# Optimization experiments

Hardware: AMD Instinct MI355X
Metric: run time of the kernel (lower is better)

## Reference

```python
import jax, jax.numpy as jnp
import numpy as np

B, S, HID = 2, 1024, 4096
NH, NKV, HD = 32, 8, 128
GROUPS = NH // NKV  # 4
BITS = 8
SCALING = HD ** -0.5


def quantize_lastdim(x, bits=BITS):
    """Asymmetric min-max fake-quant per row of the last dim (groupsize=-1),
    matching ActQuantizer.find_params + quantize/dequantize."""
    qmax = float(2 ** bits - 1)
    xmin = jnp.minimum(jnp.min(x, axis=-1, keepdims=True), 0.0)
    xmax = jnp.maximum(jnp.max(x, axis=-1, keepdims=True), 0.0)
    rng = xmax - xmin
    scale = jnp.where(rng == 0, 1.0, rng / qmax)
    zero = jnp.round(-xmin / scale)
    q = jnp.clip(jnp.round(x / scale) + zero, 0.0, qmax)
    return (q - zero) * scale


def rotate_half(x):
    x1, x2 = jnp.split(x, 2, axis=-1)
    return jnp.concatenate([-x2, x1], axis=-1)


def setup_inputs() -> dict:
    key = jax.random.key(0)
    ks = jax.random.split(key, 5)
    hidden_states = jax.random.normal(ks[0], (B, S, HID), dtype=jnp.float32)
    w_std = 0.02
    Wq = w_std * jax.random.normal(ks[1], (NH * HD, HID), dtype=jnp.float32)
    Wk = w_std * jax.random.normal(ks[2], (NKV * HD, HID), dtype=jnp.float32)
    Wv = w_std * jax.random.normal(ks[3], (NKV * HD, HID), dtype=jnp.float32)
    Wo = w_std * jax.random.normal(ks[4], (HID, NH * HD), dtype=jnp.float32)
    # RoPE tables (theta=10000)
    inv_freq = 1.0 / (10000.0 ** (jnp.arange(0, HD, 2, dtype=jnp.float32) / HD))
    freqs = jnp.outer(jnp.arange(S, dtype=jnp.float32), inv_freq)  # [S, HD/2]
    emb = jnp.concatenate([freqs, freqs], axis=-1)  # [S, HD]
    cos = jnp.broadcast_to(jnp.cos(emb)[None], (B, S, HD)).astype(jnp.float32)
    sin = jnp.broadcast_to(jnp.sin(emb)[None], (B, S, HD)).astype(jnp.float32)
    # additive causal mask [B,1,S,S]
    causal = jnp.tril(jnp.ones((S, S), dtype=bool))
    attention_mask = jnp.where(causal, 0.0, -1e9).astype(jnp.float32)
    attention_mask = jnp.broadcast_to(attention_mask[None, None], (B, 1, S, S))
    return {"hidden_states": hidden_states, "cos": cos, "sin": sin,
            "attention_mask": attention_mask, "Wq": Wq, "Wk": Wk, "Wv": Wv, "Wo": Wo}


def reference(hidden_states, cos, sin, attention_mask, Wq, Wk, Wv, Wo):
    b, s, _ = hidden_states.shape
    # projections -> [B, H, S, D]
    q = (hidden_states @ Wq.T).reshape(b, s, NH, HD).transpose(0, 2, 1, 3)
    k = (hidden_states @ Wk.T).reshape(b, s, NKV, HD).transpose(0, 2, 1, 3)
    v = (hidden_states @ Wv.T).reshape(b, s, NKV, HD).transpose(0, 2, 1, 3)
    # RoPE (HF: unsqueeze cos/sin at head dim)
    c = cos[:, None, :, :]
    si = sin[:, None, :, :]
    q = q * c + rotate_half(q) * si
    k = k * c + rotate_half(k) * si
    # SmoothK per-channel: subtract per-channel mean over the sequence
    # (softmax-invariant outlier smoothing of K before quantization)
    k = k - jnp.mean(k, axis=2, keepdims=True)
    # activation fake-quant of Q, K (per token over head_dim)
    q = quantize_lastdim(q)
    k = quantize_lastdim(k)
    # V quantized along the sequence axis (module transposes dims 2,3 first)
    v = quantize_lastdim(v.transpose(0, 1, 3, 2)).transpose(0, 1, 3, 2)
    # GQA repeat
    k_rep = jnp.repeat(k, GROUPS, axis=1)
    v_rep = jnp.repeat(v, GROUPS, axis=1)
    scores = jnp.einsum('bhqd,bhkd->bhqk', q, k_rep) * SCALING + attention_mask
    w = jax.nn.softmax(scores.astype(jnp.float32), axis=-1).astype(q.dtype)
    # fake-quant attention weights per row (groupsize=-1, so no padding)
    w = quantize_lastdim(w)
    attn = jnp.einsum('bhqk,bhkd->bhqd', w, v_rep)
    attn = attn.transpose(0, 2, 1, 3).reshape(b, s, NH * HD)
    out = attn @ Wo.T
    return (out, w)
```

## Files before the change

### kernel.cpp

```cpp
#include <hip/hip_runtime.h>
#include <math.h>
#include <stdint.h>

typedef unsigned int u32;
typedef unsigned short u16;
typedef __bf16 bf16x8 __attribute__((ext_vector_type(8)));
typedef float f32x4 __attribute__((ext_vector_type(4)));
typedef unsigned short u16x8 __attribute__((ext_vector_type(8)));
typedef unsigned short u16x4 __attribute__((ext_vector_type(4)));

constexpr int   Bb  = 2;
constexpr int   Ss  = 1024;
constexpr int   HID = 4096;
constexpr int   NH  = 32;
constexpr int   NKV = 8;
constexpr int   HD  = 128;
constexpr float SCALING = 0.0883883476483184405501f;

enum { M_QKV = 0, M_OUT = 3 };

__device__ __forceinline__ u16 f2bf(float f) {
  u32 u = __builtin_bit_cast(u32, f);
  u = u + 0x7fffu + ((u >> 16) & 1u);
  return (u16)(u >> 16);
}

__device__ __forceinline__ void gld_lds16(const void* g, void* l) {
  __builtin_amdgcn_global_load_lds(
      (const __attribute__((address_space(1))) u32*)(uintptr_t)g,
      (__attribute__((address_space(3))) u32*)(uintptr_t)l, 16, 0, 0);
}

template <int MODE>
__global__ __launch_bounds__(256) void mfma_gemm(
    const u16* __restrict__ Abf_g,
    const u16* __restrict__ B0, const u16* __restrict__ B1,
    const u16* __restrict__ B2,
    float* __restrict__ Cf, float* __restrict__ Ck, float* __restrict__ Cv,
    int K) {
  __shared__ u16 As[128 * 32];
  __shared__ u16 Bs[128 * 32];

  const int tid = threadIdx.x;
  const int lane = tid & 63;
  const int wid = tid >> 6;
  const int wr = wid >> 1, wc = wid & 1;

  const int m0 = blockIdx.y * 128;
  int nloc = blockIdx.x * 128;

  const u16* Abf = Abf_g + (size_t)m0 * K;
  const u16* Bp = nullptr;
  int which = 0;

  if (MODE == M_QKV) {
    const int j = blockIdx.x;
    if (j < 32)      { which = 0; Bp = B0 + (size_t)j * 128 * K;        nloc = j * 128; }
    else if (j < 40) { which = 1; Bp = B1 + (size_t)(j - 32) * 128 * K; nloc = (j - 32) * 128; }
    else             { which = 2; Bp = B2 + (size_t)(j - 40) * 128 * K; nloc = (j - 40) * 128; }
  } else {
    Bp = B0 + (size_t)nloc * K;
  }

  f32x4 acc[4][4];
#pragma unroll
  for (int i = 0; i < 4; i++)
#pragma unroll
    for (int j = 0; j < 4; j++) acc[i][j] = (f32x4){0.f, 0.f, 0.f, 0.f};

  const int sr = lane >> 2;
  const int sp = lane & 3;
  const int fr = lane & 15;
  const int fq = lane >> 4;

  for (int kt = 0; kt < K; kt += 32) {
    __syncthreads();
#pragma unroll
    for (int cc = 0; cc < 2; ++cc) {
      const int c = wid + cc * 4;
      const int r = c * 16 + sr;
      const int sw = (r >> 1) & 3;
      const u16* ga = Abf + (size_t)r * K + kt + ((sp ^ sw) * 8);
      gld_lds16(ga, &As[c * 512]);
      const u16* gb = Bp + (size_t)r * K + kt + ((sp ^ sw) * 8);
      gld_lds16(gb, &Bs[c * 512]);
    }
    __syncthreads();

    bf16x8 av[4], bv[4];
#pragma unroll
    for (int f = 0; f < 4; ++f) {
      const int ra = wr * 64 + f * 16 + fr;
      av[f] = *(const bf16x8*)&As[ra * 32 + ((fq ^ ((ra >> 1) & 3)) * 8)];
      const int rb = wc * 64 + f * 16 + fr;
      bv[f] = *(const bf16x8*)&Bs[rb * 32 + ((fq ^ ((rb >> 1) & 3)) * 8)];
    }
#pragma unroll
    for (int i = 0; i < 4; i++)
#pragma unroll
      for (int j = 0; j < 4; j++)
        acc[i][j] = __builtin_amdgcn_mfma_f32_16x16x32_bf16(av[i], bv[j], acc[i][j], 0, 0, 0);
  }

#pragma unroll
  for (int i = 0; i < 4; i++) {
#pragma unroll
    for (int j = 0; j < 4; j++) {
      const int n = nloc + wc * 64 + j * 16 + fr;
#pragma unroll
      for (int e = 0; e < 4; e++) {
        const int m = m0 + wr * 64 + i * 16 + fq * 4 + e;
        float val = acc[i][j][e];
        if (MODE == M_QKV) {
          const int b = m >> 10, s = m & 1023, h = n >> 7, d = n & 127;
          if (which == 0)      Cf[((size_t)(b * NH + h) * Ss + s) * HD + d] = val;
          else if (which == 1) Ck[((size_t)(b * NKV + h) * Ss + s) * HD + d] = val;
          else                 Cv[((size_t)(b * NKV + h) * HD + d) * Ss + s] = val;
        } else {
          Cf[(size_t)m * HID + n] = val;
        }
      }
    }
  }
}

__global__ __launch_bounds__(256) void fused_attn(
    const u16* __restrict__ qb,
    const u16* __restrict__ kb,
    const u16* __restrict__ vTb,
    float* __restrict__ wout,
    u16* __restrict__ attnb) {
  __shared__ u16 Ks[64 * 128];
  __shared__ u16 Vs[128 * 64];
  __shared__ u16 plds[4][16 * 64];
  __shared__ float scl_l[4][16];

  const int a = 15 - (int)(blockIdx.x >> 6);
  const int bh = blockIdx.x & 63;
  const int b = bh >> 5, h = bh & 31;
  const int kv = h >> 2;
  const int tid = threadIdx.x;
  const int lane = tid & 63;
  const int wq = tid >> 6;
  const int fr = lane & 15, fq = lane >> 4;

  const int nt = a + 1;
  const int Q0 = a * 64;
  const int qw0 = Q0 + wq * 16;

  const u16* Kb = kb + (size_t)(b * NKV + kv) * Ss * HD;
  const u16* Vb = vTb + (size_t)(b * NKV + kv) * HD * Ss;
  float* wrow = wout + (size_t)bh * Ss * Ss;

  if (a < 15) {
    const int base = 64 * nt;
    const int n4 = 16 * (15 - a);
#pragma unroll
    for (int r0 = 0; r0 < 4; ++r0) {
      const int row = Q0 + r0 * 16 + (tid >> 4);
      float4* wp = (float4*)&wrow[(size_t)row * Ss + base];
      for (int c = tid & 15; c < n4; c += 16) wp[c] = float4{0.f, 0.f, 0.f, 0.f};
    }
  }

  bf16x8 qf[4];
#pragma unroll
  for (int kk = 0; kk < 4; kk++)
    qf[kk] = *(const bf16x8*)&qb[((size_t)bh * Ss + qw0 + fr) * HD + kk * 32 + fq * 8];

  float m[4], l[4];
#pragma unroll
  for (int i = 0; i < 4; i++) { m[i] = -1e30f; l[i] = 0.f; }

  for (int t = 0; t < nt; ++t) {
    __syncthreads();
#pragma unroll
    for (int c = 0; c < 4; ++c) {
      const int idx0 = (c * 4 + wq) * 64;
      const int idx = idx0 + lane;
      const int row = idx >> 4, sl = idx & 15;
      const int slot = sl ^ (row & 15);
      gld_lds16(Kb + (size_t)(t * 64 + row) * HD + slot * 8, &Ks[idx0 * 8]);
    }
    __syncthreads();

    f32x4 sa[4];
#pragma unroll
    for (int jn = 0; jn < 4; jn++) sa[jn] = (f32x4){0.f, 0.f, 0.f, 0.f};
#pragma unroll
    for (int kk = 0; kk < 4; ++kk) {
      bf16x8 kfv[4];
#pragma unroll
      for (int jn = 0; jn < 4; ++jn) {
        const int row = jn * 16 + fr;
        kfv[jn] = *(const bf16x8*)&Ks[row * 128 + (((kk * 4 + fq) ^ fr) * 8)];
      }
#pragma unroll
      for (int jn = 0; jn < 4; ++jn)
        sa[jn] = __builtin_amdgcn_mfma_f32_16x16x32_bf16(qf[kk], kfv[jn], sa[jn], 0, 0, 0);
    }

    const bool diag = (t == a);
#pragma unroll
    for (int e = 0; e < 4; ++e) {
      const int qrow = qw0 + fq * 4 + e;
      float sv[4];
      float rmax = -1e30f;
#pragma unroll
      for (int jn = 0; jn < 4; ++jn) {
        float s = sa[jn][e] * SCALING;
        if (diag && (t * 64 + jn * 16 + fr > qrow)) s = -1e30f;
        sv[jn] = s;
        rmax = fmaxf(rmax, s);
      }
#pragma unroll
      for (int o = 1; o < 16; o <<= 1) rmax = fmaxf(rmax, __shfl_xor(rmax, o));
      const float mn = fmaxf(m[e], rmax);
      const float cc = __expf(m[e] - mn);
      float rs = __expf(sv[0] - mn) + __expf(sv[1] - mn) +
                 __expf(sv[2] - mn) + __expf(sv[3] - mn);
#pragma unroll
      for (int o = 1; o < 16; o <<= 1) rs += __shfl_xor(rs, o);
      l[e] = l[e] * cc + rs;
      m[e] = mn;
    }
  }

  float scl[4];
#pragma unroll
  for (int e = 0; e < 4; e++) scl[e] = 1.f / (255.f * l[e]);
  if (fr == 0) {
#pragma unroll
    for (int e = 0; e < 4; e++) scl_l[wq][fq * 4 + e] = scl[e];
  }

  f32x4 acc2[8];
#pragma unroll
  for (int j = 0; j < 8; j++) acc2[j] = (f32x4){0.f, 0.f, 0.f, 0.f};

  u16* pl = &plds[wq][0];
  const int wrrow = lane >> 2, wrq = lane & 3;
  const float sclr = scl_l[wq][wrrow];

  for (int t = 0; t < nt; ++t) {
    __syncthreads();
#pragma unroll
    for (int c = 0; c < 4; ++c) {
      const int idx0 = (c * 4 + wq) * 64;
      const int idx = idx0 + lane;
      {
        const int row = idx >> 4, sl = idx & 15;
        const int slot = sl ^ (row & 15);
        gld_lds16(Kb + (size_t)(t * 64 + row) * HD + slot * 8, &Ks[idx0 * 8]);
      }
      {
        const int d = idx >> 3, sl = idx & 7;
        const int slot = sl ^ (d & 7);
        gld_lds16(Vb + (size_t)d * Ss + t * 64 + slot * 8, &Vs[idx0 * 8]);
      }
    }
    __syncthreads();

    f32x4 sa[4];
#pragma unroll
    for (int jn = 0; jn < 4; jn++) sa[jn] = (f32x4){0.f, 0.f, 0.f, 0.f};
#pragma unroll
    for (int kk = 0; kk < 4; ++kk) {
      bf16x8 kfv[4];
#pragma unroll
      for (int jn = 0; jn < 4; ++jn) {
        const int row = jn * 16 + fr;
        kfv[jn] = *(const bf16x8*)&Ks[row * 128 + (((kk * 4 + fq) ^ fr) * 8)];
      }
#pragma unroll
      for (int jn = 0; jn < 4; ++jn)
        sa[jn] = __builtin_amdgcn_mfma_f32_16x16x32_bf16(qf[kk], kfv[jn], sa[jn], 0, 0, 0);
    }

    const bool diag = (t == a);
#pragma unroll
    for (int e = 0; e < 4; ++e) {
      const int qrow = qw0 + fq * 4 + e;
      const int r16 = fq * 4 + e;
#pragma unroll
      for (int jn = 0; jn < 4; ++jn) {
        const int kc = t * 64 + jn * 16 + fr;
        float qv = 0.f;
        if (!diag || kc <= qrow)
          qv = rintf(fminf(255.f * __expf(sa[jn][e] * SCALING - m[e]), 255.f));
        const int col = jn * 16 + fr;
        const int byte = r16 * 128 + (((col >> 3) ^ (r16 & 7)) * 16) + (col & 7) * 2;
        *(u16*)((char*)pl + byte) = f2bf(qv);
      }
    }

    {
      const int s0 = (2 * wrq) ^ (wrrow & 7);
      const int s1 = (2 * wrq + 1) ^ (wrrow & 7);
      bf16x8 p0 = *(const bf16x8*)((char*)pl + wrrow * 128 + s0 * 16);
      bf16x8 p1 = *(const bf16x8*)((char*)pl + wrrow * 128 + s1 * 16);
      float* wp = &wrow[(size_t)(qw0 + wrrow) * Ss + t * 64 + wrq * 16];
      float4 o0, o1, o2, o3;
      o0.x = (float)p0[0] * sclr; o0.y = (float)p0[1] * sclr;
      o0.z = (float)p0[2] * sclr; o0.w = (float)p0[3] * sclr;
      o1.x = (float)p0[4] * sclr; o1.y = (float)p0[5] * sclr;
      o1.z = (float)p0[6] * sclr; o1.w = (float)p0[7] * sclr;
      o2.x = (float)p1[0] * sclr; o2.y = (float)p1[1] * sclr;
      o2.z = (float)p1[2] * sclr; o2.w = (float)p1[3] * sclr;
      o3.x = (float)p1[4] * sclr; o3.y = (float)p1[5] * sclr;
      o3.z = (float)p1[6] * sclr; o3.w = (float)p1[7] * sclr;
      ((float4*)wp)[0] = o0; ((float4*)wp)[1] = o1;
      ((float4*)wp)[2] = o2; ((float4*)wp)[3] = o3;
    }

#pragma unroll
    for (int kk2 = 0; kk2 < 2; ++kk2) {
      const bf16x8 pa = *(const bf16x8*)((char*)pl + fr * 128 + (((kk2 * 4 + fq) ^ (fr & 7)) * 16));
#pragma unroll
      for (int jn2 = 0; jn2 < 8; ++jn2) {
        const int d = jn2 * 16 + fr;
        const bf16x8 vb = *(const bf16x8*)&Vs[d * 64 + (((kk2 * 4 + fq) ^ (d & 7)) * 8)];
        acc2[jn2] = __builtin_amdgcn_mfma_f32_16x16x32_bf16(pa, vb, acc2[jn2], 0, 0, 0);
      }
    }
  }

#pragma unroll
  for (int e = 0; e < 4; ++e) {
    const int qrow = qw0 + fq * 4 + e;
#pragma unroll
    for (int jn2 = 0; jn2 < 8; ++jn2)
      attnb[((size_t)b * Ss + qrow) * HID + h * HD + jn2 * 16 + fr] =
          f2bf(acc2[jn2][e] * scl[e]);
  }
}

__global__ __launch_bounds__(256) void f32_to_bf16_k(const float* __restrict__ in,
                                                     u16* __restrict__ out, int n8) {
  const int i = blockIdx.x * 256 + threadIdx.x;
  if (i < n8) {
    float4 a = ((const float4*)in)[2 * i];
    float4 b = ((const float4*)in)[2 * i + 1];
    u16x8 t;
    t[0] = f2bf(a.x); t[1] = f2bf(a.y); t[2] = f2bf(a.z); t[3] = f2bf(a.w);
    t[4] = f2bf(b.x); t[5] = f2bf(b.y); t[6] = f2bf(b.z); t[7] = f2bf(b.w);
    ((u16x8*)out)[i] = t;
  }
}

__global__ __launch_bounds__(256) void rope_quant_q(const float* __restrict__ q,
                                                    u16* __restrict__ qb,
                                                    const float* __restrict__ cs,
                                                    const float* __restrict__ sn) {
  const int row = blockIdx.x * 4 + (threadIdx.x >> 6);
  const int lane = threadIdx.x & 63;
  const int s = row & (Ss - 1);
  const int b = row >> 15;
  const float* p = q + (size_t)row * HD;
  const float* cp = cs + ((size_t)b * Ss + s) * HD;
  const float* sp = sn + ((size_t)b * Ss + s) * HD;
  float x1 = p[lane], x2 = p[lane + 64];
  float r1 = x1 * cp[lane] - x2 * sp[lane];
  float r2 = x2 * cp[lane + 64] + x1 * sp[lane + 64];
  float mn = fminf(0.f, fminf(r1, r2));
  float mx = fmaxf(0.f, fmaxf(r1, r2));
#pragma unroll
  for (int o = 32; o; o >>= 1) {
    mn = fminf(mn, __shfl_xor(mn, o));
    mx = fmaxf(mx, __shfl_xor(mx, o));
  }
  float rng = mx - mn;
  float scale = (rng == 0.f) ? 1.f : rng / 255.f;
  float zero = rintf(-mn / scale);
  float q1 = fminf(fmaxf(rintf(r1 / scale) + zero, 0.f), 255.f);
  float q2 = fminf(fmaxf(rintf(r2 / scale) + zero, 0.f), 255.f);
  qb[(size_t)row * HD + lane] = f2bf((q1 - zero) * scale);
  qb[(size_t)row * HD + lane + 64] = f2bf((q2 - zero) * scale);
}

__global__ __launch_bounds__(256) void rope_k(float* __restrict__ k,
                                              const float* __restrict__ cs,
                                              const float* __restrict__ sn) {
  const int row = blockIdx.x * 4 + (threadIdx.x >> 6);
  const int lane = threadIdx.x & 63;
  const int s = row & (Ss - 1);
  const int b = row >> 13;
  float* p = k + (size_t)row * HD;
  const float* cp = cs + ((size_t)b * Ss + s) * HD;
  const float* sp = sn + ((size_t)b * Ss + s) * HD;
  float x1 = p[lane], x2 = p[lane + 64];
  float r1 = x1 * cp[lane] - x2 * sp[lane];
  float r2 = x2 * cp[lane + 64] + x1 * sp[lane + 64];
  p[lane] = r1;
  p[lane + 64] = r2;
}

__global__ __launch_bounds__(1024) void kmean_kernel(const float* __restrict__ k,
                                                     float* __restrict__ kmean) {
  const int bh = blockIdx.x;
  const int d = threadIdx.x & 127;
  const int sl = threadIdx.x >> 7;
  const float* p = k + (size_t)bh * Ss * HD;
  float sum = 0.f;
  for (int s = sl; s < Ss; s += 8) sum += p[(size_t)s * HD + d];
  __shared__ float lds[8][128];
  lds[sl][d] = sum;
  __syncthreads();
  if (threadIdx.x < 128) {
    float t = 0.f;
#pragma unroll
    for (int i = 0; i < 8; i++) t += lds[i][threadIdx.x];
    kmean[bh * HD + threadIdx.x] = t * (1.f / 1024.f);
  }
}

__global__ __launch_bounds__(256) void k_subquant(const float* __restrict__ k,
                                                  u16* __restrict__ kb,
                                                  const float* __restrict__ kmean) {
  const int row = blockIdx.x * 4 + (threadIdx.x >> 6);
  const int lane = threadIdx.x & 63;
  const int bh = row >> 10;
  const float* p = k + (size_t)row * HD;
  float x1 = p[lane] - kmean[bh * HD + lane];
  float x2 = p[lane + 64] - kmean[bh * HD + lane + 64];
  float mn = fminf(0.f, fminf(x1, x2));
  float mx = fmaxf(0.f, fmaxf(x1, x2));
#pragma unroll
  for (int o = 32; o; o >>= 1) {
    mn = fminf(mn, __shfl_xor(mn, o));
    mx = fmaxf(mx, __shfl_xor(mx, o));
  }
  float rng = mx - mn;
  float scale = (rng == 0.f) ? 1.f : rng / 255.f;
  float zero = rintf(-mn / scale);
  float q1 = fminf(fmaxf(rintf(x1 / scale) + zero, 0.f), 255.f);
  float q2 = fminf(fmaxf(rintf(x2 / scale) + zero, 0.f), 255.f);
  kb[(size_t)row * HD + lane] = f2bf((q1 - zero) * scale);
  kb[(size_t)row * HD + lane + 64] = f2bf((q2 - zero) * scale);
}

__global__ __launch_bounds__(256) void vquant(const float* __restrict__ vT,
                                              u16* __restrict__ vTb) {
  const float* p = vT + (size_t)blockIdx.x * Ss;
  const int t = threadIdx.x;
  float4 x = ((const float4*)p)[t];
  float mn = fminf(0.f, fminf(fminf(x.x, x.y), fminf(x.z, x.w)));
  float mx = fmaxf(0.f, fmaxf(fmaxf(x.x, x.y), fmaxf(x.z, x.w)));
#pragma unroll
  for (int o = 32; o; o >>= 1) {
    mn = fminf(mn, __shfl_xor(mn, o));
    mx = fmaxf(mx, __shfl_xor(mx, o));
  }
  __shared__ float smn[4], smx[4];
  const int wid = t >> 6, lane = t & 63;
  if (lane == 0) { smn[wid] = mn; smx[wid] = mx; }
  __syncthreads();
  mn = fminf(fminf(smn[0], smn[1]), fminf(smn[2], smn[3]));
  mx = fmaxf(fmaxf(smx[0], smx[1]), fmaxf(smx[2], smx[3]));
  float rng = mx - mn;
  float scale = (rng == 0.f) ? 1.f : rng / 255.f;
  float zero = rintf(-mn / scale);
  u16x4 o4;
  o4[0] = f2bf((fminf(fmaxf(rintf(x.x / scale) + zero, 0.f), 255.f) - zero) * scale);
  o4[1] = f2bf((fminf(fmaxf(rintf(x.y / scale) + zero, 0.f), 255.f) - zero) * scale);
  o4[2] = f2bf((fminf(fmaxf(rintf(x.z / scale) + zero, 0.f), 255.f) - zero) * scale);
  o4[3] = f2bf((fminf(fmaxf(rintf(x.w / scale) + zero, 0.f), 255.f) - zero) * scale);
  ((u16x4*)vTb)[(size_t)blockIdx.x * 256 + t] = o4;
}

extern "C" void kernel_launch(void* const* d_in, const int* in_sizes, int n_in,
                              void* d_out, int out_size, void* d_ws, size_t ws_size,
                              hipStream_t stream) {
  const float* hs = (const float*)d_in[0];
  const float* cosp = (const float*)d_in[1];
  const float* sinp = (const float*)d_in[2];
  const float* Wq = (const float*)d_in[4];
  const float* Wk = (const float*)d_in[5];
  const float* Wv = (const float*)d_in[6];
  const float* Wo = (const float*)d_in[7];

  float* out = (float*)d_out;
  float* wout = out + (size_t)Bb * Ss * HID;

  char* wsp = (char*)d_ws;
  auto alloc = [&](size_t bytes) {
    char* p = wsp;
    wsp += (bytes + 255) & ~(size_t)255;
    return p;
  };
  float* q     = (float*)alloc((size_t)Bb * NH * Ss * HD * 4);
  float* k     = (float*)alloc((size_t)Bb * NKV * Ss * HD * 4);
  float* vT    = (float*)alloc((size_t)Bb * NKV * Ss * HD * 4);
  float* kmean = (float*)alloc((size_t)Bb * NKV * HD * 4);
  u16* hsb = (u16*)alloc((size_t)Bb * Ss * HID * 2);
  u16* qb  = (u16*)alloc((size_t)Bb * NH * Ss * HD * 2);
  u16* kb  = (u16*)alloc((size_t)Bb * NKV * Ss * HD * 2);
  u16* vTb = (u16*)alloc((size_t)Bb * NKV * Ss * HD * 2);
  u16* Wqb = (u16*)alloc((size_t)NH * HD * HID * 2);
  u16* Wkb = (u16*)alloc((size_t)NKV * HD * HID * 2);
  u16* Wvb = (u16*)alloc((size_t)NKV * HD * HID * 2);
  u16* Wob = (u16*)alloc((size_t)HID * NH * HD * 2);
  u16* attnb = (u16*)q;

  f32_to_bf16_k<<<(Bb * Ss * HID / 8 + 255) / 256, 256, 0, stream>>>(hs, hsb, Bb * Ss * HID / 8);
  f32_to_bf16_k<<<(NH * HD * HID / 8 + 255) / 256, 256, 0, stream>>>(Wq, Wqb, NH * HD * HID / 8);
  f32_to_bf16_k<<<(NKV * HD * HID / 8 + 255) / 256, 256, 0, stream>>>(Wk, Wkb, NKV * HD * HID / 8);
  f32_to_bf16_k<<<(NKV * HD * HID / 8 + 255) / 256, 256, 0, stream>>>(Wv, Wvb, NKV * HD * HID / 8);
  f32_to_bf16_k<<<(HID * NH * HD / 8 + 255) / 256, 256, 0, stream>>>(Wo, Wob, HID * NH * HD / 8);

  mfma_gemm<M_QKV><<<dim3(48, 16, 1), 256, 0, stream>>>(
      hsb, Wqb, Wkb, Wvb, q, k, vT, HID);

  rope_quant_q<<<(Bb * NH * Ss) / 4, 256, 0, stream>>>(q, qb, cosp, sinp);
  rope_k<<<(Bb * NKV * Ss) / 4, 256, 0, stream>>>(k, cosp, sinp);
  kmean_kernel<<<Bb * NKV, 1024, 0, stream>>>(k, kmean);
  k_subquant<<<(Bb * NKV * Ss) / 4, 256, 0, stream>>>(k, kb, kmean);
  vquant<<<Bb * NKV * HD, 256, 0, stream>>>(vT, vTb);

  fused_attn<<<dim3(1024), 256, 0, stream>>>(qb, kb, vTb, wout, attnb);

  mfma_gemm<M_OUT><<<dim3(32, 16, 1), 256, 0, stream>>>(
      attnb, Wob, nullptr, nullptr, out, nullptr, nullptr, HID);
}
```

Measured before the change: 509.7 us.

## Triple-buffer GEMM LDS tiles with async global-to-LDS prefetch two stages ahead

Converts the MFMA GEMM main loop from a single LDS buffer with two barriers per k-step into a three-stage ring buffer. Loads for step k+2 are issued before computing step k, and explicit vmcnt waits plus a single barrier per iteration keep the stages in order. MFMA issue priority is raised with s_setprio. This is meant to hide global memory latency behind MFMA work, at the cost of three times the LDS per block and a launch-bounds hint that caps register use.

```diff
diff --git a/kernel.cpp b/kernel.cpp
--- a/kernel.cpp
+++ b/kernel.cpp
@@ -32,14 +32,14 @@
 }
 
 template <int MODE>
-__global__ __launch_bounds__(256) void mfma_gemm(
+__global__ __launch_bounds__(256, 3) void mfma_gemm(
     const u16* __restrict__ Abf_g,
     const u16* __restrict__ B0, const u16* __restrict__ B1,
     const u16* __restrict__ B2,
     float* __restrict__ Cf, float* __restrict__ Ck, float* __restrict__ Cv,
     int K) {
-  __shared__ u16 As[128 * 32];
-  __shared__ u16 Bs[128 * 32];
+  __shared__ u16 As[3][128 * 32];
+  __shared__ u16 Bs[3][128 * 32];
 
   const int tid = threadIdx.x;
   const int lane = tid & 63;
@@ -73,33 +73,62 @@
   const int fr = lane & 15;
   const int fq = lane >> 4;
 
-  for (int kt = 0; kt < K; kt += 32) {
-    __syncthreads();
+  const int nk = K >> 5;
+
+#pragma unroll
+  for (int p = 0; p < 2; ++p) {
 #pragma unroll
     for (int cc = 0; cc < 2; ++cc) {
       const int c = wid + cc * 4;
       const int r = c * 16 + sr;
-      const int sw = (r >> 1) & 3;
-      const u16* ga = Abf + (size_t)r * K + kt + ((sp ^ sw) * 8);
-      gld_lds16(ga, &As[c * 512]);
-      const u16* gb = Bp + (size_t)r * K + kt + ((sp ^ sw) * 8);
-      gld_lds16(gb, &Bs[c * 512]);
-    }
-    __syncthreads();
+      const int go = (sp ^ ((r >> 1) & 3)) * 8;
+      gld_lds16(Abf + (size_t)r * K + p * 32 + go, &As[p][c * 512]);
+      gld_lds16(Bp + (size_t)r * K + p * 32 + go, &Bs[p][c * 512]);
+    }
+  }
+  asm volatile("s_waitcnt vmcnt(4)" ::: "memory");
+  __builtin_amdgcn_sched_barrier(0);
+  __builtin_amdgcn_s_barrier();
+
+  int cur = 0;
+  for (int kt = 0; kt < nk; ++kt) {
+    if (kt + 2 < nk) {
+      const int stg = (cur == 0) ? 2 : cur - 1;
+#pragma unroll
+      for (int cc = 0; cc < 2; ++cc) {
+        const int c = wid + cc * 4;
+        const int r = c * 16 + sr;
+        const int go = (sp ^ ((r >> 1) & 3)) * 8;
+        gld_lds16(Abf + (size_t)r * K + (kt + 2) * 32 + go, &As[stg][c * 512]);
+        gld_lds16(Bp + (size_t)r * K + (kt + 2) * 32 + go, &Bs[stg][c * 512]);
+      }
+    }
 
     bf16x8 av[4], bv[4];
 #pragma unroll
     for (int f = 0; f < 4; ++f) {
       const int ra = wr * 64 + f * 16 + fr;
-      av[f] = *(const bf16x8*)&As[ra * 32 + ((fq ^ ((ra >> 1) & 3)) * 8)];
+      av[f] = *(const bf16x8*)&As[cur][ra * 32 + ((fq ^ ((ra >> 1) & 3)) * 8)];
       const int rb = wc * 64 + f * 16 + fr;
-      bv[f] = *(const bf16x8*)&Bs[rb * 32 + ((fq ^ ((rb >> 1) & 3)) * 8)];
-    }
+      bv[f] = *(const bf16x8*)&Bs[cur][rb * 32 + ((fq ^ ((rb >> 1) & 3)) * 8)];
+    }
+
+    __builtin_amdgcn_s_setprio(1);
 #pragma unroll
     for (int i = 0; i < 4; i++)
 #pragma unroll
       for (int j = 0; j < 4; j++)
         acc[i][j] = __builtin_amdgcn_mfma_f32_16x16x32_bf16(av[i], bv[j], acc[i][j], 0, 0, 0);
+    __builtin_amdgcn_s_setprio(0);
+
+    if (kt + 2 < nk) {
+      asm volatile("s_waitcnt vmcnt(4)" ::: "memory");
+    } else {
+      asm volatile("s_waitcnt vmcnt(0)" ::: "memory");
+    }
+    __builtin_amdgcn_sched_barrier(0);
+    __builtin_amdgcn_s_barrier();
+    cur = (cur == 2) ? 0 : cur + 1;
   }
 
 #pragma unroll
```

Result: faster. 453.9 us (-10.9%).
